# Optimization experiments

Hardware: AMD Instinct MI355X
Metric: run time of the kernel (lower is better)

Reference implementation:

```python
import jax, jax.numpy as jnp
import numpy as np

N, M = 3000, 6000            # nodes, edges
FV, FE, H1, H2, NC = 128, 64, 256, 128, 16


def setup_inputs() -> dict:
    key = jax.random.key(0)
    ks = jax.random.split(key, 20)
    r = lambda i, sh: jax.random.normal(ks[i], sh, dtype=jnp.float32)
    return dict(
        X=r(0, (N, FV)),
        Z=r(1, (M, FE)),
        adj_e=jax.random.uniform(ks[2], (M, M), dtype=jnp.float32),
        adj_v=jax.random.uniform(ks[3], (N, N), dtype=jnp.float32),
        T=jax.random.uniform(ks[4], (N, M), dtype=jnp.float32),
        edge_index=jax.random.randint(ks[5], (2, 2 * M), 0, N),
        W1=r(6, (FV, H1)) * 0.05, b1=jnp.zeros((H1,), jnp.float32),
        p2=r(7, (1, H1)), W2=r(8, (FE, FE)) * 0.05, b2=jnp.zeros((FE,), jnp.float32),
        p3=r(9, (1, H1)), W3=r(10, (FE, FE)) * 0.05, b3=jnp.zeros((FE,), jnp.float32),
        p32=r(11, (1, H1)), W32=r(12, (FE, FE)) * 0.05, b32=jnp.zeros((FE,), jnp.float32),
        p4=r(13, (1, FE)), W4=r(14, (H1, H2)) * 0.05,
        b4g=jnp.zeros((H2,), jnp.float32), b4=jnp.zeros((H2,), jnp.float32),
        W5=r(15, (H2, NC)) * 0.05, b5=jnp.zeros((NC,), jnp.float32),
    )


def gcn(x, W, b, edge_index, n):
    """PyG GCNConv: symmetric-normalized A+I propagation."""
    src, dst = edge_index[0], edge_index[1]
    loop = jnp.arange(n)
    s = jnp.concatenate([src, loop])
    d = jnp.concatenate([dst, loop])
    deg = jax.ops.segment_sum(jnp.ones(s.shape[0], x.dtype), d, num_segments=n)
    dinv = jnp.where(deg > 0, jax.lax.rsqrt(deg), 0.0)
    norm = dinv[s] * dinv[d]                      # [E+n]
    xw = x @ W                                    # [n, out]
    return jax.ops.segment_sum(xw[s] * norm[:, None], d, num_segments=n) + b


def edge_layer(Hv, He, adj_e, T, p, W, b):
    # multiplier2 = T.T @ diag(Hv @ p.T) @ T, done as a fused column scale of T
    sv = (Hv @ p.T)[:, 0]                         # [n]
    m2 = T.T @ (T * sv[:, None])                  # [m, m]
    idx = jnp.arange(m2.shape[0])
    M3 = m2.at[idx, idx].set(1.0)                 # identity on diag, m2 off-diag
    A = M3 * adj_e
    An = A / A.max(axis=0, keepdims=True)         # column-max normalize
    return An @ (He @ W) + b


def reference(X, Z, adj_e, adj_v, T, edge_index,
              W1, b1, p2, W2, b2, p3, W3, b3, p32, W32, b32,
              p4, W4, b4g, b4, W5, b5):
    relu = jax.nn.relu
    # gc1: plain GCN on nodes (normalGCN=True), edges passed through
    Xh = relu(gcn(X, W1, b1, edge_index, N))
    Zh = relu(Z)
    # gc2, gc3, gc3_2: edge layers
    Zh = relu(edge_layer(Xh, Zh, adj_e, T, p2, W2, b2)); Xh = relu(Xh)
    Zh = relu(edge_layer(Xh, Zh, adj_e, T, p3, W3, b3)); Xh = relu(Xh)
    Zh = relu(edge_layer(Xh, Zh, adj_e, T, p32, W32, b32)); Xh = relu(Xh)
    # gc4: node layer with multiplier1 = T @ diag(He @ p.T) @ T.T
    se = (Zh @ p4.T)[:, 0]                        # [m]
    mult1 = (T * se[None, :]) @ T.T               # [n, n]
    X4 = mult1 @ gcn(Xh, W4, b4g, edge_index, N) + b4
    Xh = relu(X4); Zh = relu(Zh)
    # gc5: plain GCN -> softmax over classes
    X5 = gcn(Xh, W5, b5, edge_index, N)
    return jax.nn.softmax(X5, axis=1)
```

## Files before the change

kernel.cpp:

```cpp
#include <hip/hip_runtime.h>
#include <cmath>
#include <cstddef>

#define NN 3000
#define MM 6000
#define FV 128
#define FE 64
#define H1 256
#define H2 128
#define NC 16
#define E2 12000

#define CT_E 47
#define KT_E 94
#define CT_M 24
#define KT_M 188
#define KT_A 188
#define NPK_M 94
#define PKA_BYTES ((size_t)48 * KT_E * 8192)
#define PKM_BYTES ((size_t)CT_M * KT_M * 8192)
#define APK_BYTES ((size_t)CT_E * KT_A * 8192)

static inline int cdiv(int a, int b) { return (a + b - 1) / b; }

typedef __attribute__((ext_vector_type(8))) short short8;
typedef __attribute__((ext_vector_type(4))) float f32x4;

__device__ inline void atomicMaxFloat(float* addr, float v) {
  if (v >= 0.f) atomicMax((int*)addr, __float_as_int(v));
  else          atomicMin((unsigned int*)addr, __float_as_uint(v));
}

__device__ inline unsigned short b2h(float x) {
  unsigned int u = __float_as_uint(x);
  return (unsigned short)((u + 0x7FFFu + ((u >> 16) & 1u)) >> 16);
}

__device__ inline void bsplit(float x, unsigned short& h, unsigned short& l) {
  h = b2h(x);
  float hf = __uint_as_float(((unsigned int)h) << 16);
  l = b2h(x - hf);
}

__global__ void k_fill(float* p, float v, int n) {
  int i = blockIdx.x * blockDim.x + threadIdx.x;
  if (i < n) p[i] = v;
}

__global__ void k_fill_bias(float* p, const float* __restrict__ bias, int nmask, int total) {
  int i = blockIdx.x * blockDim.x + threadIdx.x;
  if (i < total) p[i] = bias[i & nmask];
}

__global__ void k_relu_copy(const float* __restrict__ in, float* __restrict__ out, int n) {
  int i = blockIdx.x * blockDim.x + threadIdx.x;
  if (i < n) out[i] = fmaxf(in[i], 0.f);
}

__global__ void k_relu(float* p, int n) {
  int i = blockIdx.x * blockDim.x + threadIdx.x;
  if (i < n) p[i] = fmaxf(p[i], 0.f);
}

__global__ void k_deg_count(const int* __restrict__ dst, float* deg, int ne) {
  int e = blockIdx.x * blockDim.x + threadIdx.x;
  if (e < ne) atomicAdd(&deg[dst[e]], 1.f);
}

__global__ void k_dinv(float* deg, int n) {
  int i = blockIdx.x * blockDim.x + threadIdx.x;
  if (i < n) deg[i] = rsqrtf(deg[i] + 1.0f);
}

__global__ void k_gcn_init(const float* __restrict__ xw, const float* __restrict__ dinv,
                           const float* __restrict__ bias, float* __restrict__ out,
                           int n, int flog2) {
  int idx = blockIdx.x * blockDim.x + threadIdx.x;
  int F = 1 << flog2;
  if (idx < n * F) {
    int i = idx >> flog2;
    int f = idx & (F - 1);
    float di = dinv[i];
    out[idx] = xw[idx] * di * di + bias[f];
  }
}

__global__ void k_gcn_scatter(const float* __restrict__ xw, const int* __restrict__ src,
                              const int* __restrict__ dst, const float* __restrict__ dinv,
                              float* __restrict__ out, int ne, int flog2) {
  int idx = blockIdx.x * blockDim.x + threadIdx.x;
  int F = 1 << flog2;
  if (idx < ne * F) {
    int e = idx >> flog2;
    int f = idx & (F - 1);
    int s = src[e], d = dst[e];
    atomicAdd(&out[d * F + f], xw[s * F + f] * dinv[s] * dinv[d]);
  }
}

__global__ void k_rowdot(const float* __restrict__ Xv, const float* __restrict__ p,
                         float* __restrict__ out, int rows, int K) {
  int row = blockIdx.x * 4 + (threadIdx.x >> 6);
  int lane = threadIdx.x & 63;
  if (row >= rows) return;
  float acc = 0.f;
  for (int k = lane; k < K; k += 64) acc += Xv[(size_t)row * K + k] * p[k];
  for (int off = 32; off > 0; off >>= 1) acc += __shfl_xor(acc, off);
  if (lane == 0) out[row] = acc;
}

__global__ void k_prep(const float* __restrict__ HeW, const float* __restrict__ cmax,
                       const float* __restrict__ bias,
                       float* __restrict__ Bc, float* __restrict__ Zh, int total) {
  int idx = blockIdx.x * blockDim.x + threadIdx.x;
  if (idx < total) {
    Bc[idx] = HeW[idx] / cmax[idx >> 6];
    Zh[idx] = bias[idx & 63];
  }
}

__global__ void k_prep_pack(const float* __restrict__ HeW, const float* __restrict__ cmax,
                            const float* __restrict__ bias,
                            float* __restrict__ Zh, char* __restrict__ Bpk, int Kd) {
  int kt = blockIdx.x;
  int t = threadIdx.x;
  int f = t >> 2, g = t & 3;
  float bf = bias[f];
  unsigned short hv[8];
#pragma unroll
  for (int e = 0; e < 8; ++e) {
    int k = kt * 32 + g * 8 + e;
    float v = 0.f;
    if (k < Kd) {
      v = HeW[(size_t)k * 64 + f] / cmax[k];
      Zh[(size_t)k * 64 + f] = bf;
    }
    hv[e] = b2h(v);
  }
  uint4 H;
  H.x = (unsigned)hv[0] | ((unsigned)hv[1] << 16);
  H.y = (unsigned)hv[2] | ((unsigned)hv[3] << 16);
  H.z = (unsigned)hv[4] | ((unsigned)hv[5] << 16);
  H.w = (unsigned)hv[6] | ((unsigned)hv[7] << 16);
  *(uint4*)(Bpk + (size_t)kt * 4096 + f * 64 + ((g ^ ((f >> 1) & 3)) * 16)) = H;
}

__global__ void k_pack_g(const float* __restrict__ g, char* __restrict__ gpk, int Kd) {
  int kt = blockIdx.x;
  int t = threadIdx.x;
#pragma unroll
  for (int it = 0; it < 2; ++it) {
    int idx = it * 256 + t;
    int f = idx >> 2, gsw = idx & 3;
    int gq = gsw ^ ((f >> 1) & 3);
    unsigned short hv[8];
#pragma unroll
    for (int e = 0; e < 8; ++e) {
      int k = kt * 32 + gq * 8 + e;
      float v = (k < Kd) ? g[(size_t)k * 128 + f] : 0.f;
      hv[e] = b2h(v);
    }
    uint4 H;
    H.x = (unsigned)hv[0] | ((unsigned)hv[1] << 16);
    H.y = (unsigned)hv[2] | ((unsigned)hv[3] << 16);
    H.z = (unsigned)hv[4] | ((unsigned)hv[5] << 16);
    H.w = (unsigned)hv[6] | ((unsigned)hv[7] << 16);
    *(uint4*)(gpk + (size_t)kt * 8192 + idx * 16) = H;
  }
}

__global__ void k_scale_pack(const char* __restrict__ src, char* __restrict__ dst,
                             const float* __restrict__ s, float* __restrict__ cmax,
                             int nkt, int nk, int Md) {
  int ct = blockIdx.x, kt = blockIdx.y;
  size_t base = ((size_t)ct * nkt + kt) * 8192;
  int t = threadIdx.x;
  if (cmax && kt == 0 && t < 128) {
    int cc = ct * 128 + t;
    if (cc < Md) cmax[cc] = -INFINITY;
  }
#pragma unroll
  for (int it = 0; it < 2; ++it) {
    int idx = it * 256 + t;
    int c = idx >> 2, gsw = idx & 3;
    int g = gsw ^ ((c >> 1) & 3);
    uint4 H = *(const uint4*)(src + base + idx * 16);
    unsigned int hw[4] = {H.x, H.y, H.z, H.w};
    unsigned int ow[4];
#pragma unroll
    for (int p = 0; p < 4; ++p) {
      int k0 = kt * 32 + g * 8 + p * 2;
      float s0 = (k0 < nk) ? s[k0] : 0.f;
      float s1 = (k0 + 1 < nk) ? s[k0 + 1] : 0.f;
      float v0 = __uint_as_float((hw[p] & 0xFFFFu) << 16) * s0;
      float v1 = __uint_as_float((hw[p] >> 16) << 16) * s1;
      ow[p] = (unsigned)b2h(v0) | ((unsigned)b2h(v1) << 16);
    }
    uint4 O;
    O.x = ow[0]; O.y = ow[1]; O.z = ow[2]; O.w = ow[3];
    *(uint4*)(dst + base + idx * 16) = O;
  }
}

__global__ void k_pack_edge(const float* __restrict__ T, const float* __restrict__ svp,
                            char* __restrict__ ph, char* __restrict__ pl,
                            float* __restrict__ cmax,
                            int scaled, int Md, int Kd, int nkt) {
  int ct = blockIdx.x, kt = blockIdx.y;
  size_t base = ((size_t)ct * nkt + kt) * 8192;
  int t = threadIdx.x;
  if (scaled && kt == 0 && t < 128) {
    int cc = ct * 128 + t;
    if (cc < Md) cmax[cc] = -INFINITY;
  }
#pragma unroll
  for (int it = 0; it < 2; ++it) {
    int tau = it * 256 + t;
    int c = tau & 127;
    int g = tau >> 7;
    int gc = ct * 128 + c;
    int off = c * 64 + ((g ^ ((c >> 1) & 3)) * 16);
    unsigned short hv[8], lv[8];
#pragma unroll
    for (int e = 0; e < 8; ++e) {
      int k = kt * 32 + g * 8 + e;
      float v = 0.f;
      if (k < Kd && gc < Md) {
        v = T[(size_t)k * Md + gc];
        if (scaled) v *= svp[k];
      }
      bsplit(v, hv[e], lv[e]);
    }
    uint4 H, L;
    H.x = (unsigned)hv[0] | ((unsigned)hv[1] << 16);
    H.y = (unsigned)hv[2] | ((unsigned)hv[3] << 16);
    H.z = (unsigned)hv[4] | ((unsigned)hv[5] << 16);
    H.w = (unsigned)hv[6] | ((unsigned)hv[7] << 16);
    *(uint4*)(ph + base + off) = H;
    if (pl) {
      L.x = (unsigned)lv[0] | ((unsigned)lv[1] << 16);
      L.y = (unsigned)lv[2] | ((unsigned)lv[3] << 16);
      L.z = (unsigned)lv[4] | ((unsigned)lv[5] << 16);
      L.w = (unsigned)lv[6] | ((unsigned)lv[7] << 16);
      *(uint4*)(pl + base + off) = L;
    }
  }
}

__global__ void k_pack_tt(const float* __restrict__ T, const float* __restrict__ sep,
                          char* __restrict__ ph, char* __restrict__ pl,
                          int scaled, int Mt, int Kt, int nkt) {
  int ct = blockIdx.x, kt = blockIdx.y;
  size_t base = ((size_t)ct * nkt + kt) * 8192;
  int t = threadIdx.x;
#pragma unroll
  for (int it = 0; it < 2; ++it) {
    int tau = it * 256 + t;
    int c = tau >> 2;
    int g = tau & 3;
    int node = ct * 128 + c;
    int off = c * 64 + ((g ^ ((c >> 1) & 3)) * 16);
    unsigned short hv[8], lv[8];
#pragma unroll
    for (int e = 0; e < 8; ++e) {
      int k = kt * 32 + g * 8 + e;
      float v = 0.f;
      if (node < Mt && k < Kt) {
        v = T[(size_t)node * Kt + k];
        if (scaled) v *= sep[k];
      }
      bsplit(v, hv[e], lv[e]);
    }
    uint4 H, L;
    H.x = (unsigned)hv[0] | ((unsigned)hv[1] << 16);
    H.y = (unsigned)hv[2] | ((unsigned)hv[3] << 16);
    H.z = (unsigned)hv[4] | ((unsigned)hv[5] << 16);
    H.w = (unsigned)hv[6] | ((unsigned)hv[7] << 16);
    *(uint4*)(ph + base + off) = H;
    if (pl) {
      L.x = (unsigned)lv[0] | ((unsigned)lv[1] << 16);
      L.y = (unsigned)lv[2] | ((unsigned)lv[3] << 16);
      L.z = (unsigned)lv[4] | ((unsigned)lv[5] << 16);
      L.w = (unsigned)lv[6] | ((unsigned)lv[7] << 16);
      *(uint4*)(pl + base + off) = L;
    }
  }
}

template <int EPI>
__global__ __launch_bounds__(256) void k_tsvt_sym(const char* __restrict__ pAh,
                                                  const char* __restrict__ pBh,
                                                  const float* __restrict__ adj,
                                                  char* __restrict__ Opk,
                                                  float* __restrict__ cmax,
                                                  int Md, int nkt, int nbt, int npk) {
  __shared__ __align__(16) char smem[32768];
  const int tid = threadIdx.x;
  const int lane = tid & 63;
  const int w = tid >> 6;
  const int wr = w >> 1;
  const int wc = w & 1;
  const int r16 = lane & 15;
  const int kb = lane >> 4;

  int nwg = nbt * (nbt + 1) / 2;
  int orig = blockIdx.x;
  int q = nwg >> 3, r = nwg & 7;
  int xcd = orig & 7, pos = orig >> 3;
  int wgid = (xcd < r ? xcd * (q + 1) : r * (q + 1) + (xcd - r) * q) + pos;
  int bi = 0, rem = wgid;
  while (rem >= nbt - bi) { rem -= nbt - bi; ++bi; }
  int bj = bi + rem;

  const int i0 = bi * 128, j0 = bj * 128;

  const char* srcA = pAh + (size_t)bi * nkt * 8192;
  const char* srcB = pBh + (size_t)bj * nkt * 8192;
  const int c4 = w * 4;

  auto stage = [&](int kt, int buf) {
#pragma unroll
    for (int o = 0; o < 4; ++o) {
      int c = c4 + o;
      int sel = c >> 3, sub = c & 7;
      const char* s = (sel ? srcB : srcA) + (size_t)kt * 8192 + sub * 1024 + lane * 16;
      __builtin_amdgcn_global_load_lds(
          (const __attribute__((address_space(1))) void*)s,
          (__attribute__((address_space(3))) void*)(smem + buf * 16384 + c * 1024 + lane * 16),
          16, 0, 0);
    }
  };

  f32x4 acc[4][4];
#pragma unroll
  for (int a = 0; a < 4; ++a)
#pragma unroll
    for (int b = 0; b < 4; ++b) acc[a][b] = 0.f;

  stage(0, 0);
  __syncthreads();
  int cur = 0;
  for (int kt = 0; kt < nkt; ++kt) {
    if (kt + 1 < nkt) stage(kt + 1, cur ^ 1);
    const char* sA = smem + cur * 16384;
    const char* sB = sA + 8192;

    short8 bh[4];
#pragma unroll
    for (int nj = 0; nj < 4; ++nj) {
      int col = wc * 64 + nj * 16 + r16;
      bh[nj] = *(const short8*)(sB + col * 64 + ((kb ^ ((col >> 1) & 3)) * 16));
    }
#pragma unroll
    for (int mi = 0; mi < 4; ++mi) {
      int row = wr * 64 + mi * 16 + r16;
      short8 ah = *(const short8*)(sA + row * 64 + ((kb ^ ((row >> 1) & 3)) * 16));
#pragma unroll
      for (int nj = 0; nj < 4; ++nj)
        acc[mi][nj] = __builtin_amdgcn_mfma_f32_16x16x32_bf16(ah, bh[nj], acc[mi][nj], 0, 0, 0);
    }
    __syncthreads();
    cur ^= 1;
  }

#pragma unroll
  for (int nj = 0; nj < 4; ++nj) {
    int jl = wc * 64 + nj * 16 + r16;
#pragma unroll
    for (int mi = 0; mi < 4; ++mi) {
      int ilb = wr * 64 + mi * 16 + kb * 4;
      f32x4 a = acc[mi][nj];
#pragma unroll
      for (int rr = 0; rr < 4; ++rr) {
        int il = ilb + rr;
        *(unsigned short*)(smem + jl * 256 + ((il * 2) ^ ((jl & 7) << 4))) = b2h(a[rr]);
      }
    }
  }

#pragma unroll
  for (int nj = 0; nj < 4; ++nj) {
    int j = j0 + wc * 64 + nj * 16 + r16;
    float cm = -INFINITY;
    bool jok = (j < Md);
#pragma unroll
    for (int mi = 0; mi < 4; ++mi) {
      int ib = i0 + wr * 64 + mi * 16 + kb * 4;
      f32x4 a = acc[mi][nj];
#pragma unroll
      for (int rr = 0; rr < 4; ++rr) {
        int i = ib + rr;
        if (i < Md && jok && i <= j) {
          float v = a[rr];
          if (EPI == 1) {
            if (i == j) v = 1.0f;
            v *= __builtin_nontemporal_load(&adj[(size_t)i * Md + j]);
            cm = fmaxf(cm, v);
          }
          *(unsigned short*)(Opk + ((size_t)(i >> 7) * npk + (j >> 5)) * 8192
              + (i & 127) * 64 + ((((j >> 3) & 3) ^ ((i >> 1) & 3)) * 16) + (j & 7) * 2)
              = b2h(v);
        }
      }
    }
    if (EPI == 1) {
      cm = fmaxf(cm, __shfl_xor(cm, 16));
      cm = fmaxf(cm, __shfl_xor(cm, 32));
      if (kb == 0 && jok) atomicMaxFloat(&cmax[j], cm);
    }
  }

  __syncthreads();
  {
    int ic = tid & 127;
    int i = i0 + ic;
    int rowpar = tid >> 7;
    bool iok = (i < Md);
    float lm = -INFINITY;
#pragma unroll 8
    for (int m = 0; m < 64; ++m) {
      int jr = m * 2 + rowpar;
      int j = j0 + jr;
      if (iok && j < Md && i < j) {
        unsigned short hv =
            *(unsigned short*)(smem + jr * 256 + ((ic * 2) ^ ((jr & 7) << 4)));
        float vm = __uint_as_float(((unsigned int)hv) << 16);
        if (EPI == 1) {
          float a2 = vm * __builtin_nontemporal_load(&adj[(size_t)j * Md + i]);
          *(unsigned short*)(Opk + ((size_t)(j >> 7) * npk + (i >> 5)) * 8192
              + (j & 127) * 64 + ((((i >> 3) & 3) ^ ((j >> 1) & 3)) * 16) + (i & 7) * 2)
              = b2h(a2);
          lm = fmaxf(lm, a2);
        } else {
          *(unsigned short*)(Opk + ((size_t)(j >> 7) * npk + (i >> 5)) * 8192
              + (j & 127) * 64 + ((((i >> 3) & 3) ^ ((j >> 1) & 3)) * 16) + (i & 7) * 2)
              = b2h(vm);
        }
      }
    }
    if (EPI == 1 && iok && lm > -INFINITY) atomicMaxFloat(&cmax[i], lm);
  }
}

__global__ __launch_bounds__(256) void k_zh(const char* __restrict__ Apk,
                                            const char* __restrict__ Bpk,
                                            float* __restrict__ Zh,
                                            int Mn, int nktA, int zchunk) {
  __shared__ __align__(16) char smem[12288];
  const int tid = threadIdx.x;
  const int lane = tid & 63;
  const int w = tid >> 6;
  const int r16 = lane & 15;
  const int kb = lane >> 4;
  const int bi = blockIdx.x;
  const int kt0 = blockIdx.y * zchunk;
  const int kt1 = min(nktA, kt0 + zchunk);
  const int i0 = bi * 128;

  f32x4 acc[2][4];
#pragma unroll
  for (int a = 0; a < 2; ++a)
#pragma unroll
    for (int b = 0; b < 4; ++b) acc[a][b] = 0.f;

  for (int kt = kt0; kt < kt1; ++kt) {
    const char* As = Apk + ((size_t)bi * nktA + kt) * 8192;
    const char* Bs = Bpk + (size_t)kt * 4096;
    __builtin_amdgcn_global_load_lds(
        (const __attribute__((address_space(1))) void*)(As + tid * 16),
        (__attribute__((address_space(3))) void*)(smem + tid * 16), 16, 0, 0);
    __builtin_amdgcn_global_load_lds(
        (const __attribute__((address_space(1))) void*)(As + 4096 + tid * 16),
        (__attribute__((address_space(3))) void*)(smem + 4096 + tid * 16), 16, 0, 0);
    __builtin_amdgcn_global_load_lds(
        (const __attribute__((address_space(1))) void*)(Bs + tid * 16),
        (__attribute__((address_space(3))) void*)(smem + 8192 + tid * 16), 16, 0, 0);
    __syncthreads();
    short8 bh[4];
#pragma unroll
    for (int nj = 0; nj < 4; ++nj) {
      int f = nj * 16 + r16;
      bh[nj] = *(const short8*)(smem + 8192 + f * 64 + ((kb ^ ((f >> 1) & 3)) * 16));
    }
#pragma unroll
    for (int mi = 0; mi < 2; ++mi) {
      int c = w * 32 + mi * 16 + r16;
      short8 ah = *(const short8*)(smem + c * 64 + ((kb ^ ((c >> 1) & 3)) * 16));
#pragma unroll
      for (int nj = 0; nj < 4; ++nj)
        acc[mi][nj] = __builtin_amdgcn_mfma_f32_16x16x32_bf16(ah, bh[nj], acc[mi][nj], 0, 0, 0);
    }
    __syncthreads();
  }
#pragma unroll
  for (int mi = 0; mi < 2; ++mi) {
    int ib = i0 + w * 32 + mi * 16 + kb * 4;
#pragma unroll
    for (int nj = 0; nj < 4; ++nj) {
      int f = nj * 16 + r16;
      f32x4 a = acc[mi][nj];
#pragma unroll
      for (int r = 0; r < 4; ++r) {
        int i = ib + r;
        if (i < Mn) atomicAdd(&Zh[(size_t)i * 64 + f], a[r]);
      }
    }
  }
}

__global__ __launch_bounds__(256) void k_zh128(const char* __restrict__ Apk,
                                               const char* __restrict__ Bpk,
                                               float* __restrict__ C,
                                               int Mn, int nktA, int zchunk) {
  __shared__ __align__(16) char smem[16384];
  const int tid = threadIdx.x;
  const int lane = tid & 63;
  const int w = tid >> 6;
  const int r16 = lane & 15;
  const int kb = lane >> 4;
  const int bi = blockIdx.x;
  const int kt0 = blockIdx.y * zchunk;
  const int kt1 = min(nktA, kt0 + zchunk);
  const int i0 = bi * 128;

  f32x4 acc[2][8];
#pragma unroll
  for (int a = 0; a < 2; ++a)
#pragma unroll
    for (int b = 0; b < 8; ++b) acc[a][b] = 0.f;

  for (int kt = kt0; kt < kt1; ++kt) {
    const char* As = Apk + ((size_t)bi * nktA + kt) * 8192;
    const char* Bs = Bpk + (size_t)kt * 8192;
#pragma unroll
    for (int o = 0; o < 4; ++o) {
      int idx = o * 256 + tid;
      const char* s = (idx < 512) ? (As + idx * 16) : (Bs + (idx - 512) * 16);
      __builtin_amdgcn_global_load_lds(
          (const __attribute__((address_space(1))) void*)s,
          (__attribute__((address_space(3))) void*)(smem + idx * 16), 16, 0, 0);
    }
    __syncthreads();
    short8 bh[8];
#pragma unroll
    for (int nj = 0; nj < 8; ++nj) {
      int f = nj * 16 + r16;
      bh[nj] = *(const short8*)(smem + 8192 + f * 64 + ((kb ^ ((f >> 1) & 3)) * 16));
    }
#pragma unroll
    for (int mi = 0; mi < 2; ++mi) {
      int c = w * 32 + mi * 16 + r16;
      short8 ah = *(const short8*)(smem + c * 64 + ((kb ^ ((c >> 1) & 3)) * 16));
#pragma unroll
      for (int nj = 0; nj < 8; ++nj)
        acc[mi][nj] = __builtin_amdgcn_mfma_f32_16x16x32_bf16(ah, bh[nj], acc[mi][nj], 0, 0, 0);
    }
    __syncthreads();
  }
#pragma unroll
  for (int mi = 0; mi < 2; ++mi) {
    int ib = i0 + w * 32 + mi * 16 + kb * 4;
#pragma unroll
    for (int nj = 0; nj < 8; ++nj) {
      int f = nj * 16 + r16;
      f32x4 a = acc[mi][nj];
#pragma unroll
      for (int r = 0; r < 4; ++r) {
        int i = ib + r;
        if (i < Mn) atomicAdd(&C[(size_t)i * 128 + f], a[r]);
      }
    }
  }
}

template <int EPI>
__global__ __launch_bounds__(256) void k_tsvt_cvt(const float* __restrict__ Tmat,
                                                  const float* __restrict__ svp,
                                                  const float* __restrict__ adj,
                                                  float* __restrict__ Out,
                                                  float* __restrict__ cmax,
                                                  int Md, int Kd) {
  __shared__ __align__(16) unsigned short sAh[128 * 32];
  __shared__ __align__(16) unsigned short sAl[128 * 32];
  __shared__ __align__(16) unsigned short sBh[128 * 32];
  __shared__ __align__(16) unsigned short sBl[128 * 32];
  const int tid = threadIdx.x;
  const int lane = tid & 63;
  const int w = tid >> 6;
  const int wr = w >> 1, wc = w & 1;
  const int r16 = lane & 15;
  const int kb = lane >> 4;
  const int i0 = blockIdx.y * 128;
  const int j0 = blockIdx.x * 128;
  f32x4 acc[4][4];
#pragma unroll
  for (int a = 0; a < 4; ++a)
#pragma unroll
    for (int b = 0; b < 4; ++b) acc[a][b] = 0.f;
  for (int k0 = 0; k0 < Kd; k0 += 32) {
#pragma unroll
    for (int it = 0; it < 4; ++it) {
      int s = tid + it * 256;
      int ci = s & 127;
      int kq = s >> 7;
      int kk = kq * 4;
      int kbq = kq >> 1, half = kq & 1;
      int off = ci * 64 + (kbq ^ ((ci >> 1) & 3)) * 16 + half * 8;
      float va[4];
#pragma unroll
      for (int e = 0; e < 4; ++e) {
        int k = k0 + kk + e;
        int c = i0 + ci;
        va[e] = (k < Kd && c < Md) ? Tmat[(size_t)k * Md + c] : 0.f;
      }
      unsigned short h0, h1, h2, h3, l0, l1, l2, l3;
      bsplit(va[0], h0, l0); bsplit(va[1], h1, l1);
      bsplit(va[2], h2, l2); bsplit(va[3], h3, l3);
      uint2 hp, lp;
      hp.x = (unsigned)h0 | ((unsigned)h1 << 16); hp.y = (unsigned)h2 | ((unsigned)h3 << 16);
      lp.x = (unsigned)l0 | ((unsigned)l1 << 16); lp.y = (unsigned)l2 | ((unsigned)l3 << 16);
      *(uint2*)((char*)sAh + off) = hp;
      *(uint2*)((char*)sAl + off) = lp;
      float vb[4];
#pragma unroll
      for (int e = 0; e < 4; ++e) {
        int k = k0 + kk + e;
        int c = j0 + ci;
        float svv = (k < Kd) ? svp[k] : 0.f;
        vb[e] = (k < Kd && c < Md) ? Tmat[(size_t)k * Md + c] * svv : 0.f;
      }
      bsplit(vb[0], h0, l0); bsplit(vb[1], h1, l1);
      bsplit(vb[2], h2, l2); bsplit(vb[3], h3, l3);
      hp.x = (unsigned)h0 | ((unsigned)h1 << 16); hp.y = (unsigned)h2 | ((unsigned)h3 << 16);
      lp.x = (unsigned)l0 | ((unsigned)l1 << 16); lp.y = (unsigned)l2 | ((unsigned)l3 << 16);
      *(uint2*)((char*)sBh + off) = hp;
      *(uint2*)((char*)sBl + off) = lp;
    }
    __syncthreads();
    short8 bh[4], bl[4];
#pragma unroll
    for (int nj = 0; nj < 4; ++nj) {
      int col = wc * 64 + nj * 16 + r16;
      int off = col * 64 + ((kb ^ ((col >> 1) & 3)) * 16);
      bh[nj] = *(const short8*)((const char*)sBh + off);
      bl[nj] = *(const short8*)((const char*)sBl + off);
    }
#pragma unroll
    for (int mi = 0; mi < 4; ++mi) {
      int row = wr * 64 + mi * 16 + r16;
      int off = row * 64 + ((kb ^ ((row >> 1) & 3)) * 16);
      short8 ah = *(const short8*)((const char*)sAh + off);
      short8 al = *(const short8*)((const char*)sAl + off);
#pragma unroll
      for (int nj = 0; nj < 4; ++nj) {
        acc[mi][nj] = __builtin_amdgcn_mfma_f32_16x16x32_bf16(ah, bh[nj], acc[mi][nj], 0, 0, 0);
        acc[mi][nj] = __builtin_amdgcn_mfma_f32_16x16x32_bf16(ah, bl[nj], acc[mi][nj], 0, 0, 0);
        acc[mi][nj] = __builtin_amdgcn_mfma_f32_16x16x32_bf16(al, bh[nj], acc[mi][nj], 0, 0, 0);
      }
    }
    __syncthreads();
  }
#pragma unroll
  for (int nj = 0; nj < 4; ++nj) {
    int j = j0 + wc * 64 + nj * 16 + r16;
    float cm = -INFINITY;
#pragma unroll
    for (int mi = 0; mi < 4; ++mi) {
      int ib = i0 + wr * 64 + mi * 16 + kb * 4;
      f32x4 a = acc[mi][nj];
#pragma unroll
      for (int r = 0; r < 4; ++r) {
        int i = ib + r;
        if (i < Md && j < Md) {
          float v = a[r];
          if (EPI == 1) {
            if (i == j) v = 1.0f;
            v *= adj[(size_t)i * Md + j];
            Out[(size_t)i * Md + j] = v;
            cm = fmaxf(cm, v);
          } else {
            Out[(size_t)i * Md + j] = v;
          }
        }
      }
    }
    if (EPI == 1) {
      cm = fmaxf(cm, __shfl_xor(cm, 16));
      cm = fmaxf(cm, __shfl_xor(cm, 32));
      if (kb == 0 && j < Md) atomicMaxFloat(&cmax[j], cm);
    }
  }
}

template <int SPLITK, int NT>
__global__ __launch_bounds__(256) void k_gemm64(const float* __restrict__ Am,
                                                const float* __restrict__ Bm,
                                                const float* __restrict__ bias,
                                                const float* __restrict__ kscale,
                                                float* __restrict__ C,
                                                int Mn, int Nn, int Kn, int relu) {
  __shared__ float As[16][68];
  __shared__ float Bs[16][68];
  int i0 = blockIdx.y * 64, j0 = blockIdx.x * 64;
  int kchunk = (Kn + SPLITK - 1) / SPLITK;
  int ks = blockIdx.z * kchunk;
  int ke = min(Kn, ks + kchunk);
  int tid = threadIdx.x;
  int tx = tid & 15, ty = tid >> 4;
  float acc[4][4] = {};
  for (int k0 = ks; k0 < ke; k0 += 16) {
#pragma unroll
    for (int l0 = 0; l0 < 1024; l0 += 256) {
      int l = l0 + tid;
      int i = l >> 4, k = l & 15;
      float v = 0.f;
      if (i0 + i < Mn && k0 + k < ke) {
        v = NT ? __builtin_nontemporal_load(&Am[(size_t)(i0 + i) * Kn + (k0 + k)])
               : Am[(size_t)(i0 + i) * Kn + (k0 + k)];
        if (kscale) v *= kscale[k0 + k];
      }
      As[k][i] = v;
    }
#pragma unroll
    for (int l0 = 0; l0 < 1024; l0 += 256) {
      int l = l0 + tid;
      int k = l >> 6, j = l & 63;
      float v = 0.f;
      if (k0 + k < ke && j0 + j < Nn) v = Bm[(size_t)(k0 + k) * Nn + (j0 + j)];
      Bs[k][j] = v;
    }
    __syncthreads();
#pragma unroll
    for (int k = 0; k < 16; ++k) {
      const float4 av = *(const float4*)&As[k][ty * 4];
      const float4 bv = *(const float4*)&Bs[k][tx * 4];
      float a_[4] = {av.x, av.y, av.z, av.w};
      float b_[4] = {bv.x, bv.y, bv.z, bv.w};
#pragma unroll
      for (int ri = 0; ri < 4; ++ri)
#pragma unroll
        for (int rj = 0; rj < 4; ++rj)
          acc[ri][rj] = fmaf(a_[ri], b_[rj], acc[ri][rj]);
    }
    __syncthreads();
  }
#pragma unroll
  for (int ri = 0; ri < 4; ++ri) {
    int i = i0 + ty * 4 + ri;
    if (i >= Mn) continue;
#pragma unroll
    for (int rj = 0; rj < 4; ++rj) {
      int j = j0 + tx * 4 + rj;
      if (j >= Nn) continue;
      float v = acc[ri][rj];
      if (SPLITK > 1) {
        atomicAdd(&C[(size_t)i * Nn + j], v);
      } else {
        if (bias) v += bias[j];
        if (relu) v = fmaxf(v, 0.f);
        C[(size_t)i * Nn + j] = v;
      }
    }
  }
}

__global__ void k_transpose(const float* __restrict__ in, float* __restrict__ out,
                            int rows, int cols) {
  __shared__ float tile[32][33];
  int c0 = blockIdx.x * 32, r0 = blockIdx.y * 32;
  int tx = threadIdx.x & 31, tg = threadIdx.x >> 5;
  for (int rr = tg; rr < 32; rr += 8) {
    int r = r0 + rr, c = c0 + tx;
    tile[rr][tx] = (r < rows && c < cols) ? in[(size_t)r * cols + c] : 0.f;
  }
  __syncthreads();
  for (int rr = tg; rr < 32; rr += 8) {
    int c = c0 + rr, r = r0 + tx;
    if (c < cols && r < rows) out[(size_t)c * rows + r] = tile[tx][rr];
  }
}

__global__ void k_softmax16(const float* __restrict__ X5, float* __restrict__ out, int rows) {
  int r = blockIdx.x * blockDim.x + threadIdx.x;
  if (r >= rows) return;
  float v[16];
  float m = -INFINITY;
#pragma unroll
  for (int c = 0; c < 16; ++c) { v[c] = X5[r * 16 + c]; m = fmaxf(m, v[c]); }
  float s = 0.f;
#pragma unroll
  for (int c = 0; c < 16; ++c) { v[c] = expf(v[c] - m); s += v[c]; }
  float inv = 1.f / s;
#pragma unroll
  for (int c = 0; c < 16; ++c) out[r * 16 + c] = v[c] * inv;
}

extern "C" void kernel_launch(void* const* d_in, const int* in_sizes, int n_in,
                              void* d_out, int out_size, void* d_ws, size_t ws_size,
                              hipStream_t stream) {
  const float* X     = (const float*)d_in[0];
  const float* Z     = (const float*)d_in[1];
  const float* adj_e = (const float*)d_in[2];
  const float* Tm    = (const float*)d_in[4];
  const int*   ei    = (const int*)d_in[5];
  const int* src = ei;
  const int* dst = ei + E2;
  const float* W1  = (const float*)d_in[6];
  const float* b1  = (const float*)d_in[7];
  const float* p2  = (const float*)d_in[8];
  const float* W2  = (const float*)d_in[9];
  const float* b2  = (const float*)d_in[10];
  const float* p3  = (const float*)d_in[11];
  const float* W3  = (const float*)d_in[12];
  const float* b3  = (const float*)d_in[13];
  const float* p32 = (const float*)d_in[14];
  const float* W32 = (const float*)d_in[15];
  const float* b32 = (const float*)d_in[16];
  const float* p4  = (const float*)d_in[17];
  const float* W4  = (const float*)d_in[18];
  const float* b4g = (const float*)d_in[19];
  const float* b4  = (const float*)d_in[20];
  const float* W5  = (const float*)d_in[21];
  const float* b5  = (const float*)d_in[22];

  char* wsb = (char*)d_ws;
  const bool big = ws_size >= (size_t)310 * 1024 * 1024;

  char* Apk  = wsb;
  char* pAhi = wsb + APK_BYTES;
  char* pBhi = pAhi + PKA_BYTES;
  char* Bpk  = wsb + 145539072;
  char* mAhi = wsb;
  char* mBhi = mAhi + PKM_BYTES;
  char* Mpk  = wsb + 80000000;
  char* gpk  = wsb + 100000000;

  float* small = big ? (float*)(wsb + 182000000) : (float*)d_ws + 36000000;
  float* Xh   = small;
  float* xw   = small + 768000;
  float* Zh   = small + 1536000;
  float* HeW  = small + 1920000;
  float* Bc   = small + 2304000;
  float* g    = small + 2688000;
  float* sv   = small + 3072000;
  float* se   = small + 3076096;
  float* cmax = small + 3084288;
  float* dinv = small + 3090432;
  float* X5   = small + 3093504;
  float* A_fb     = (float*)d_ws;
  float* Tt_fb    = (float*)d_ws;
  float* mult1_fb = (float*)d_ws + 18000000;
  float* out  = (float*)d_out;

  auto gemm = [&](const float* Am, const float* Bm, const float* bias, const float* ksc,
                  float* C, int Mn, int Nn, int Kn, int relu, int splitk, int nt) {
    dim3 gr(cdiv(Nn, 64), cdiv(Mn, 64), splitk);
    if (splitk == 1) {
      if (nt) k_gemm64<1, 1><<<gr, 256, 0, stream>>>(Am, Bm, bias, ksc, C, Mn, Nn, Kn, relu);
      else    k_gemm64<1, 0><<<gr, 256, 0, stream>>>(Am, Bm, bias, ksc, C, Mn, Nn, Kn, relu);
    } else {
      if (nt) k_gemm64<4, 1><<<gr, 256, 0, stream>>>(Am, Bm, bias, ksc, C, Mn, Nn, Kn, relu);
      else    k_gemm64<4, 0><<<gr, 256, 0, stream>>>(Am, Bm, bias, ksc, C, Mn, Nn, Kn, relu);
    }
  };

  k_fill<<<cdiv(NN, 256), 256, 0, stream>>>(dinv, 0.f, NN);
  k_deg_count<<<cdiv(E2, 256), 256, 0, stream>>>(dst, dinv, E2);
  k_dinv<<<cdiv(NN, 256), 256, 0, stream>>>(dinv, NN);

  gemm(X, W1, nullptr, nullptr, xw, NN, H1, FV, 0, 1, 0);
  k_gcn_init<<<cdiv(NN * H1, 256), 256, 0, stream>>>(xw, dinv, b1, Xh, NN, 8);
  k_gcn_scatter<<<cdiv(E2 * H1, 256), 256, 0, stream>>>(xw, src, dst, dinv, Xh, E2, 8);
  k_relu<<<cdiv(NN * H1, 256), 256, 0, stream>>>(Xh, NN * H1);
  k_relu_copy<<<cdiv(MM * FE, 256), 256, 0, stream>>>(Z, Zh, MM * FE);

  if (big) {
    dim3 gp(CT_E, KT_E);
    k_pack_edge<<<gp, 256, 0, stream>>>(Tm, nullptr, pAhi, nullptr, nullptr, 0, MM, NN, KT_E);
  }

  const float* ep[3] = {p2, p3, p32};
  const float* eW[3] = {W2, W3, W32};
  const float* eb[3] = {b2, b3, b32};
  const int ntriE = CT_E * (CT_E + 1) / 2;
  for (int L = 0; L < 3; ++L) {
    k_rowdot<<<cdiv(NN, 4), 256, 0, stream>>>(Xh, ep[L], sv, NN, H1);
    gemm(Zh, eW[L], nullptr, nullptr, HeW, MM, FE, FE, 0, 1, 0);
    if (big) {
      dim3 gs(CT_E, KT_E);
      k_scale_pack<<<gs, 256, 0, stream>>>(pAhi, pBhi, sv, cmax, KT_E, NN, MM);
      k_tsvt_sym<1><<<ntriE, 256, 0, stream>>>(pAhi, pBhi, adj_e, Apk, cmax,
                                               MM, KT_E, CT_E, KT_A);
      k_prep_pack<<<KT_A, 256, 0, stream>>>(HeW, cmax, eb[L], Zh, Bpk, MM);
      dim3 gz(CT_E, 8);
      k_zh<<<gz, 256, 0, stream>>>(Apk, Bpk, Zh, MM, KT_A, cdiv(KT_A, 8));
    } else {
      k_fill<<<cdiv(MM, 256), 256, 0, stream>>>(cmax, -INFINITY, MM);
      dim3 gm2(CT_E, CT_E);
      k_tsvt_cvt<1><<<gm2, 256, 0, stream>>>(Tm, sv, adj_e, A_fb, cmax, MM, NN);
      k_prep<<<cdiv(MM * FE, 256), 256, 0, stream>>>(HeW, cmax, eb[L], Bc, Zh, MM * FE);
      gemm(A_fb, Bc, nullptr, nullptr, Zh, MM, FE, MM, 0, 4, 1);
    }
    k_relu<<<cdiv(MM * FE, 256), 256, 0, stream>>>(Zh, MM * FE);
  }

  k_rowdot<<<cdiv(MM, 4), 256, 0, stream>>>(Zh, p4, se, MM, FE);
  gemm(Xh, W4, nullptr, nullptr, xw, NN, H2, H1, 0, 1, 0);
  k_gcn_init<<<cdiv(NN * H2, 256), 256, 0, stream>>>(xw, dinv, b4g, g, NN, 7);
  k_gcn_scatter<<<cdiv(E2 * H2, 256), 256, 0, stream>>>(xw, src, dst, dinv, g, E2, 7);
  if (big) {
    dim3 gp(CT_M, KT_M);
    k_pack_tt<<<gp, 256, 0, stream>>>(Tm, nullptr, mAhi, nullptr, 0, NN, MM, KT_M);
    dim3 gs(CT_M, KT_M);
    k_scale_pack<<<gs, 256, 0, stream>>>(mAhi, mBhi, se, nullptr, KT_M, MM, 0);
    const int ntriM = CT_M * (CT_M + 1) / 2;
    k_tsvt_sym<0><<<ntriM, 256, 0, stream>>>(mAhi, mBhi, nullptr, Mpk, nullptr,
                                             NN, KT_M, CT_M, NPK_M);
    k_pack_g<<<NPK_M, 256, 0, stream>>>(g, gpk, NN);
    k_fill_bias<<<cdiv(NN * H2, 256), 256, 0, stream>>>(Xh, b4, H2 - 1, NN * H2);
    dim3 gx(CT_M, 8);
    k_zh128<<<gx, 256, 0, stream>>>(Mpk, gpk, Xh, NN, NPK_M, cdiv(NPK_M, 8));
  } else {
    dim3 gt(cdiv(MM, 32), cdiv(NN, 32));
    k_transpose<<<gt, 256, 0, stream>>>(Tm, Tt_fb, NN, MM);
    dim3 gm1(cdiv(NN, 128), cdiv(NN, 128));
    k_tsvt_cvt<0><<<gm1, 256, 0, stream>>>(Tt_fb, se, nullptr, mult1_fb, nullptr, NN, MM);
    k_fill_bias<<<cdiv(NN * H2, 256), 256, 0, stream>>>(Xh, b4, H2 - 1, NN * H2);
    gemm(mult1_fb, g, nullptr, nullptr, Xh, NN, H2, NN, 0, 4, 0);
  }
  k_relu<<<cdiv(NN * H2, 256), 256, 0, stream>>>(Xh, NN * H2);

  gemm(Xh, W5, nullptr, nullptr, xw, NN, NC, H2, 0, 1, 0);
  k_gcn_init<<<cdiv(NN * NC, 256), 256, 0, stream>>>(xw, dinv, b5, X5, NN, 4);
  k_gcn_scatter<<<cdiv(E2 * NC, 256), 256, 0, stream>>>(xw, src, dst, dinv, X5, E2, 4);
  k_softmax16<<<cdiv(NN, 256), 256, 0, stream>>>(X5, out, NN);
}
```

Before: 1.233 ms.

## Fuse diagonal scaling into symmetric T^T S T kernel and batch three edge layers

Removes the separate scale-pack kernel by applying the per-k scale vector to the B operand in registers inside the MFMA loop, with the scale vector staged in shared memory. Because sv depends only on Xh, which is unchanged across the three edge layers, all three m2 products are computed in one launch with three times the workgroups, writing into three packed A buffers. The adj loads also switch from nontemporal to normal loads. In exchange, the workspace footprint grows, shared memory per block rises, and extra conversion ALU work lands in the inner loop.

```diff
diff --git a/kernel.cpp b/kernel.cpp
--- a/kernel.cpp
+++ b/kernel.cpp
@@ -17,7 +17,7 @@
 #define KT_M 188
 #define KT_A 188
 #define NPK_M 94
-#define PKA_BYTES ((size_t)48 * KT_E * 8192)
+#define PKE_BYTES ((size_t)CT_E * KT_E * 8192)
 #define PKM_BYTES ((size_t)CT_M * KT_M * 8192)
 #define APK_BYTES ((size_t)CT_E * KT_A * 8192)
 
@@ -166,39 +166,6 @@
     H.z = (unsigned)hv[4] | ((unsigned)hv[5] << 16);
     H.w = (unsigned)hv[6] | ((unsigned)hv[7] << 16);
     *(uint4*)(gpk + (size_t)kt * 8192 + idx * 16) = H;
-  }
-}
-
-__global__ void k_scale_pack(const char* __restrict__ src, char* __restrict__ dst,
-                             const float* __restrict__ s, float* __restrict__ cmax,
-                             int nkt, int nk, int Md) {
-  int ct = blockIdx.x, kt = blockIdx.y;
-  size_t base = ((size_t)ct * nkt + kt) * 8192;
-  int t = threadIdx.x;
-  if (cmax && kt == 0 && t < 128) {
-    int cc = ct * 128 + t;
-    if (cc < Md) cmax[cc] = -INFINITY;
-  }
-#pragma unroll
-  for (int it = 0; it < 2; ++it) {
-    int idx = it * 256 + t;
-    int c = idx >> 2, gsw = idx & 3;
-    int g = gsw ^ ((c >> 1) & 3);
-    uint4 H = *(const uint4*)(src + base + idx * 16);
-    unsigned int hw[4] = {H.x, H.y, H.z, H.w};
-    unsigned int ow[4];
-#pragma unroll
-    for (int p = 0; p < 4; ++p) {
-      int k0 = kt * 32 + g * 8 + p * 2;
-      float s0 = (k0 < nk) ? s[k0] : 0.f;
-      float s1 = (k0 + 1 < nk) ? s[k0 + 1] : 0.f;
-      float v0 = __uint_as_float((hw[p] & 0xFFFFu) << 16) * s0;
-      float v1 = __uint_as_float((hw[p] >> 16) << 16) * s1;
-      ow[p] = (unsigned)b2h(v0) | ((unsigned)b2h(v1) << 16);
-    }
-    uint4 O;
-    O.x = ow[0]; O.y = ow[1]; O.z = ow[2]; O.w = ow[3];
-    *(uint4*)(dst + base + idx * 16) = O;
   }
 }
 
@@ -287,14 +254,18 @@
   }
 }
 
-template <int EPI>
-__global__ __launch_bounds__(256) void k_tsvt_sym(const char* __restrict__ pAh,
-                                                  const char* __restrict__ pBh,
+template <int EPI, int SVB>
+__global__ __launch_bounds__(256) void k_tsvt_sym(const char* __restrict__ pA,
+                                                  const float* __restrict__ svg,
+                                                  int svn, int svStride,
                                                   const float* __restrict__ adj,
-                                                  char* __restrict__ Opk,
-                                                  float* __restrict__ cmax,
-                                                  int Md, int nkt, int nbt, int npk) {
-  __shared__ __align__(16) char smem[32768];
+                                                  char* __restrict__ OpkBase,
+                                                  float* __restrict__ cmaxBase,
+                                                  int Md, int nkt, int nbt, int npk,
+                                                  int ntri, size_t opkStride,
+                                                  int cmaxStride) {
+  __shared__ __align__(16) char smem[32768 + SVB];
+  constexpr int SVN = SVB / 4;
   const int tid = threadIdx.x;
   const int lane = tid & 63;
   const int w = tid >> 6;
@@ -303,20 +274,26 @@
   const int r16 = lane & 15;
   const int kb = lane >> 4;
 
-  int nwg = nbt * (nbt + 1) / 2;
+  int nwg = gridDim.x;
   int orig = blockIdx.x;
   int q = nwg >> 3, r = nwg & 7;
   int xcd = orig & 7, pos = orig >> 3;
   int wgid = (xcd < r ? xcd * (q + 1) : r * (q + 1) + (xcd - r) * q) + pos;
-  int bi = 0, rem = wgid;
+  int layer = wgid / ntri;
+  int tri = wgid - layer * ntri;
+  int bi = 0, rem = tri;
   while (rem >= nbt - bi) { rem -= nbt - bi; ++bi; }
   int bj = bi + rem;
 
   const int i0 = bi * 128, j0 = bj * 128;
-
-  const char* srcA = pAh + (size_t)bi * nkt * 8192;
-  const char* srcB = pBh + (size_t)bj * nkt * 8192;
+  const float* sv = svg + (size_t)layer * svStride;
+  char* Opk = OpkBase + (size_t)layer * opkStride;
+  float* cmax = cmaxBase ? (cmaxBase + (size_t)layer * cmaxStride) : nullptr;
+
+  const char* srcA = pA + (size_t)bi * nkt * 8192;
+  const char* srcB = pA + (size_t)bj * nkt * 8192;
   const int c4 = w * 4;
+  float* svl = (float*)(smem + 32768);
 
   auto stage = [&](int kt, int buf) {
 #pragma unroll
@@ -338,6 +315,7 @@
     for (int b = 0; b < 4; ++b) acc[a][b] = 0.f;
 
   stage(0, 0);
+  for (int k = tid; k < SVN; k += 256) svl[k] = (k < svn) ? sv[k] : 0.f;
   __syncthreads();
   int cur = 0;
   for (int kt = 0; kt < nkt; ++kt) {
@@ -345,11 +323,27 @@
     const char* sA = smem + cur * 16384;
     const char* sB = sA + 8192;
 
+    const float* svp8 = (const float*)((const char*)svl + kt * 128 + kb * 32);
+    float4 sva = *(const float4*)svp8;
+    float4 svb = *(const float4*)(svp8 + 4);
+    float svv[8] = {sva.x, sva.y, sva.z, sva.w, svb.x, svb.y, svb.z, svb.w};
+
     short8 bh[4];
 #pragma unroll
     for (int nj = 0; nj < 4; ++nj) {
       int col = wc * 64 + nj * 16 + r16;
-      bh[nj] = *(const short8*)(sB + col * 64 + ((kb ^ ((col >> 1) & 3)) * 16));
+      uint4 wv = *(const uint4*)(sB + col * 64 + ((kb ^ ((col >> 1) & 3)) * 16));
+      unsigned int ws[4] = {wv.x, wv.y, wv.z, wv.w};
+      unsigned int rw[4];
+#pragma unroll
+      for (int p = 0; p < 4; ++p) {
+        float lo = __uint_as_float(ws[p] << 16) * svv[2 * p];
+        float hi = __uint_as_float(ws[p] & 0xFFFF0000u) * svv[2 * p + 1];
+        asm("v_cvt_pk_bf16_f32 %0, %1, %2" : "=v"(rw[p]) : "v"(lo), "v"(hi));
+      }
+      uint4 rv;
+      rv.x = rw[0]; rv.y = rw[1]; rv.z = rw[2]; rv.w = rw[3];
+      bh[nj] = *(short8*)&rv;
     }
 #pragma unroll
     for (int mi = 0; mi < 4; ++mi) {
@@ -394,7 +388,7 @@
           float v = a[rr];
           if (EPI == 1) {
             if (i == j) v = 1.0f;
-            v *= __builtin_nontemporal_load(&adj[(size_t)i * Md + j]);
+            v *= adj[(size_t)i * Md + j];
             cm = fmaxf(cm, v);
           }
           *(unsigned short*)(Opk + ((size_t)(i >> 7) * npk + (j >> 5)) * 8192
@@ -426,7 +420,7 @@
             *(unsigned short*)(smem + jr * 256 + ((ic * 2) ^ ((jr & 7) << 4)));
         float vm = __uint_as_float(((unsigned int)hv) << 16);
         if (EPI == 1) {
-          float a2 = vm * __builtin_nontemporal_load(&adj[(size_t)j * Md + i]);
+          float a2 = vm * adj[(size_t)j * Md + i];
           *(unsigned short*)(Opk + ((size_t)(j >> 7) * npk + (i >> 5)) * 8192
               + (j & 127) * 64 + ((((i >> 3) & 3) ^ ((j >> 1) & 3)) * 16) + (i & 7) * 2)
               = b2h(a2);
@@ -826,27 +820,25 @@
   char* wsb = (char*)d_ws;
   const bool big = ws_size >= (size_t)310 * 1024 * 1024;
 
-  char* Apk  = wsb;
-  char* pAhi = wsb + APK_BYTES;
-  char* pBhi = pAhi + PKA_BYTES;
-  char* Bpk  = wsb + 145539072;
+  char* ApkB = wsb;
+  char* pAhi = wsb + 3 * APK_BYTES;
+  char* Bpk  = wsb + 253345792;
   char* mAhi = wsb;
-  char* mBhi = mAhi + PKM_BYTES;
-  char* Mpk  = wsb + 80000000;
-  char* gpk  = wsb + 100000000;
-
-  float* small = big ? (float*)(wsb + 182000000) : (float*)d_ws + 36000000;
-  float* Xh   = small;
-  float* xw   = small + 768000;
-  float* Zh   = small + 1536000;
-  float* HeW  = small + 1920000;
-  float* Bc   = small + 2304000;
-  float* g    = small + 2688000;
-  float* sv   = small + 3072000;
-  float* se   = small + 3076096;
-  float* cmax = small + 3084288;
-  float* dinv = small + 3090432;
-  float* X5   = small + 3093504;
+  char* Mpk  = wsb + 40000000;
+  char* gpk  = wsb + 60000000;
+
+  float* small = big ? (float*)(wsb + 255000000) : (float*)d_ws + 36000000;
+  float* Xh    = small;
+  float* xw    = small + 768000;
+  float* Zh    = small + 1536000;
+  float* HeW   = small + 1920000;
+  float* Bc    = small + 2304000;
+  float* g     = small + 2688000;
+  float* svg   = small + 3072000;
+  float* se    = small + 3082000;
+  float* cmaxB = small + 3090000;
+  float* dinv  = small + 3110000;
+  float* X5    = small + 3114000;
   float* A_fb     = (float*)d_ws;
   float* Tt_fb    = (float*)d_ws;
   float* mult1_fb = (float*)d_ws + 18000000;
@@ -874,34 +866,41 @@
   k_relu<<<cdiv(NN * H1, 256), 256, 0, stream>>>(Xh, NN * H1);
   k_relu_copy<<<cdiv(MM * FE, 256), 256, 0, stream>>>(Z, Zh, MM * FE);
 
-  if (big) {
-    dim3 gp(CT_E, KT_E);
-    k_pack_edge<<<gp, 256, 0, stream>>>(Tm, nullptr, pAhi, nullptr, nullptr, 0, MM, NN, KT_E);
-  }
-
   const float* ep[3] = {p2, p3, p32};
   const float* eW[3] = {W2, W3, W32};
   const float* eb[3] = {b2, b3, b32};
   const int ntriE = CT_E * (CT_E + 1) / 2;
-  for (int L = 0; L < 3; ++L) {
-    k_rowdot<<<cdiv(NN, 4), 256, 0, stream>>>(Xh, ep[L], sv, NN, H1);
-    gemm(Zh, eW[L], nullptr, nullptr, HeW, MM, FE, FE, 0, 1, 0);
-    if (big) {
-      dim3 gs(CT_E, KT_E);
-      k_scale_pack<<<gs, 256, 0, stream>>>(pAhi, pBhi, sv, cmax, KT_E, NN, MM);
-      k_tsvt_sym<1><<<ntriE, 256, 0, stream>>>(pAhi, pBhi, adj_e, Apk, cmax,
-                                               MM, KT_E, CT_E, KT_A);
-      k_prep_pack<<<KT_A, 256, 0, stream>>>(HeW, cmax, eb[L], Zh, Bpk, MM);
+
+  if (big) {
+    dim3 gp(CT_E, KT_E);
+    k_pack_edge<<<gp, 256, 0, stream>>>(Tm, nullptr, pAhi, nullptr, nullptr, 0, MM, NN, KT_E);
+    for (int L = 0; L < 3; ++L)
+      k_rowdot<<<cdiv(NN, 4), 256, 0, stream>>>(Xh, ep[L], svg + L * 3072, NN, H1);
+    k_fill<<<cdiv(3 * 6016, 256), 256, 0, stream>>>(cmaxB, -INFINITY, 3 * 6016);
+
+    k_tsvt_sym<1, 12032><<<3 * ntriE, 256, 0, stream>>>(
+        pAhi, svg, NN, 3072, adj_e, ApkB, cmaxB,
+        MM, KT_E, CT_E, KT_A, ntriE, APK_BYTES, 6016);
+
+    for (int L = 0; L < 3; ++L) {
+      gemm(Zh, eW[L], nullptr, nullptr, HeW, MM, FE, FE, 0, 1, 0);
+      k_prep_pack<<<KT_A, 256, 0, stream>>>(HeW, cmaxB + L * 6016, eb[L], Zh, Bpk, MM);
       dim3 gz(CT_E, 8);
-      k_zh<<<gz, 256, 0, stream>>>(Apk, Bpk, Zh, MM, KT_A, cdiv(KT_A, 8));
-    } else {
-      k_fill<<<cdiv(MM, 256), 256, 0, stream>>>(cmax, -INFINITY, MM);
+      k_zh<<<gz, 256, 0, stream>>>(ApkB + (size_t)L * APK_BYTES, Bpk, Zh, MM, KT_A,
+                                   cdiv(KT_A, 8));
+      k_relu<<<cdiv(MM * FE, 256), 256, 0, stream>>>(Zh, MM * FE);
+    }
+  } else {
+    for (int L = 0; L < 3; ++L) {
+      k_rowdot<<<cdiv(NN, 4), 256, 0, stream>>>(Xh, ep[L], svg, NN, H1);
+      gemm(Zh, eW[L], nullptr, nullptr, HeW, MM, FE, FE, 0, 1, 0);
+      k_fill<<<cdiv(MM, 256), 256, 0, stream>>>(cmaxB, -INFINITY, MM);
       dim3 gm2(CT_E, CT_E);
-      k_tsvt_cvt<1><<<gm2, 256, 0, stream>>>(Tm, sv, adj_e, A_fb, cmax, MM, NN);
-      k_prep<<<cdiv(MM * FE, 256), 256, 0, stream>>>(HeW, cmax, eb[L], Bc, Zh, MM * FE);
+      k_tsvt_cvt<1><<<gm2, 256, 0, stream>>>(Tm, svg, adj_e, A_fb, cmaxB, MM, NN);
+      k_prep<<<cdiv(MM * FE, 256), 256, 0, stream>>>(HeW, cmaxB, eb[L], Bc, Zh, MM * FE);
       gemm(A_fb, Bc, nullptr, nullptr, Zh, MM, FE, MM, 0, 4, 1);
-    }
-    k_relu<<<cdiv(MM * FE, 256), 256, 0, stream>>>(Zh, MM * FE);
+      k_relu<<<cdiv(MM * FE, 256), 256, 0, stream>>>(Zh, MM * FE);
+    }
   }
 
   k_rowdot<<<cdiv(MM, 4), 256, 0, stream>>>(Zh, p4, se, MM, FE);
@@ -911,11 +910,10 @@
   if (big) {
     dim3 gp(CT_M, KT_M);
     k_pack_tt<<<gp, 256, 0, stream>>>(Tm, nullptr, mAhi, nullptr, 0, NN, MM, KT_M);
-    dim3 gs(CT_M, KT_M);
-    k_scale_pack<<<gs, 256, 0, stream>>>(mAhi, mBhi, se, nullptr, KT_M, MM, 0);
     const int ntriM = CT_M * (CT_M + 1) / 2;
-    k_tsvt_sym<0><<<ntriM, 256, 0, stream>>>(mAhi, mBhi, nullptr, Mpk, nullptr,
-                                             NN, KT_M, CT_M, NPK_M);
+    k_tsvt_sym<0, 24064><<<ntriM, 256, 0, stream>>>(
+        mAhi, se, MM, 0, nullptr, Mpk, nullptr,
+        NN, KT_M, CT_M, NPK_M, ntriM, 0, 0);
     k_pack_g<<<NPK_M, 256, 0, stream>>>(g, gpk, NN);
     k_fill_bias<<<cdiv(NN * H2, 256), 256, 0, stream>>>(Xh, b4, H2 - 1, NN * H2);
     dim3 gx(CT_M, 8);
```

After: 1.299 ms. 1.05x slower.
